# Kernel tuning notes

Measured on AMD Instinct MI355X. Metric: run time of the kernel, lower is better.

Reference implementation:

```python
import jax, jax.numpy as jnp
import numpy as np

D_MODEL = 1024
NUM_EXPERTS = 8


def setup_inputs() -> dict:
    key = jax.random.key(0)
    k_x, k_wg, k_bg, k_we, k_be = jax.random.split(key, 5)
    B, S, D, E = 4, 2048, D_MODEL, NUM_EXPERTS
    x = jax.random.normal(k_x, (B, S, D), dtype=jnp.float32)
    # gate: nn.Linear(d_model, num_experts) -> weight [E, D], bias [E]
    Wg = jax.random.normal(k_wg, (E, D), dtype=jnp.float32) * 0.02
    bg = jax.random.normal(k_bg, (E,), dtype=jnp.float32) * 0.02
    # experts: E x nn.Linear(d_model, d_model) -> weights [E, D, D], biases [E, D]
    We = jax.random.normal(k_we, (E, D, D), dtype=jnp.float32) * 0.02
    be = jax.random.normal(k_be, (E, D), dtype=jnp.float32) * 0.02
    return {"x": x, "Wg": Wg, "bg": bg, "We": We, "be": be, "top_k": 2}


def reference(x, Wg, bg, We, be, top_k):
    # gate_scores: softmax over experts. x:[B,S,D], Wg:[E,D] -> [B,S,E]
    gate_scores = jax.nn.softmax(jnp.einsum("bsd,ed->bse", x, Wg) + bg, axis=-1)
    top_k_values, top_k_indices = jax.lax.top_k(gate_scores, top_k)  # [B,S,K]
    # dense all-expert compute (faithful to original): [B,S,D,E]
    expert_outputs = jnp.einsum("bsd,ekd->bske", x, We) + be.T  # be.T: [D,E]
    # gather top-k experts along last dim: idx broadcast over feature dim D
    top_k_outputs = jnp.take_along_axis(
        expert_outputs, top_k_indices[:, :, None, :], axis=-1
    )  # [B,S,D,K]
    weighted = (top_k_outputs * top_k_values[:, :, None, :]).sum(axis=-1)  # [B,S,D]
    return weighted
```

## Files before the change

kernel.cpp:

```cpp
#include <hip/hip_runtime.h>
#include <hip/hip_bf16.h>
#include <stdint.h>

#define D_MODEL 1024
#define NUM_EXPERTS 8
#define NBUCKET 16
#define BM 128
#define BN 128
#define BK 64
#define GATE_TOK 32

typedef __bf16 bf16x8 __attribute__((ext_vector_type(8)));
typedef float f32x4 __attribute__((ext_vector_type(4)));

__device__ __forceinline__ unsigned short f32_to_bf16_rne(float f) {
    union { float f; uint32_t u; } v;
    v.f = f;
    uint32_t u = v.u;
    u += 0x7FFFu + ((u >> 16) & 1u);
    return (unsigned short)(u >> 16);
}

__device__ __forceinline__ float bf16_to_f32(unsigned short h) {
    union { uint32_t u; float f; } v;
    v.u = ((uint32_t)h) << 16;
    return v.f;
}

__device__ __forceinline__ void gload_lds16(const unsigned short* g, unsigned short* l) {
    __builtin_amdgcn_global_load_lds(
        (const __attribute__((address_space(1))) void*)g,
        (__attribute__((address_space(3))) void*)l,
        16, 0, 0);
}

__global__ __launch_bounds__(256) void gate_kernel(
    const float* __restrict__ x, const float* __restrict__ Wg,
    const float* __restrict__ bg, int T,
    int* __restrict__ counts, int* __restrict__ token_list,
    float* __restrict__ gate_list, unsigned short* __restrict__ xb)
{
    const int tid  = threadIdx.x;
    const int lane = tid & 63;
    const int wave = tid >> 6;
    const int tokBase = blockIdx.x * GATE_TOK;

    __shared__ float4 WgS[NUM_EXPERTS * 256];
    __shared__ double logitS[GATE_TOK][NUM_EXPERTS];
    __shared__ int cntS[NBUCKET];
    __shared__ int baseS[NBUCKET];

    if (tid < NBUCKET) cntS[tid] = 0;
#pragma unroll
    for (int i = 0; i < 8; i++)
        WgS[i * 256 + tid] = ((const float4*)Wg)[i * 256 + tid];
    __syncthreads();

    for (int tt = 0; tt < GATE_TOK / 4; tt++) {
        const int lt = wave * (GATE_TOK / 4) + tt;
        const int token = tokBase + lt;
        const float4* xr4 = (const float4*)(x + (size_t)token * D_MODEL);
        ushort4* xbr4 = (ushort4*)(xb + (size_t)token * D_MODEL);

        float4 xv[4];
#pragma unroll
        for (int q = 0; q < 4; q++) {
            float4 f = xr4[q * 64 + lane];
            xv[q] = f;
            ushort4 o;
            o.x = f32_to_bf16_rne(f.x);
            o.y = f32_to_bf16_rne(f.y);
            o.z = f32_to_bf16_rne(f.z);
            o.w = f32_to_bf16_rne(f.w);
            xbr4[q * 64 + lane] = o;
        }

        double acc[NUM_EXPERTS];
#pragma unroll
        for (int e = 0; e < NUM_EXPERTS; e++) {
            double a = 0.0;
#pragma unroll
            for (int q = 0; q < 4; q++) {
                float4 w = WgS[e * 256 + q * 64 + lane];
                a += (double)xv[q].x * (double)w.x;
                a += (double)xv[q].y * (double)w.y;
                a += (double)xv[q].z * (double)w.z;
                a += (double)xv[q].w * (double)w.w;
            }
            acc[e] = a;
        }
#pragma unroll
        for (int e = 0; e < NUM_EXPERTS; e++) {
            double a = acc[e];
            for (int off = 32; off > 0; off >>= 1) a += __shfl_xor(a, off, 64);
            acc[e] = a;
        }
        if (lane == 0) {
#pragma unroll
            for (int e = 0; e < NUM_EXPERTS; e++)
                logitS[lt][e] = acc[e] + (double)bg[e];
        }
    }
    __syncthreads();

    int i1 = 0, i2 = 0, o1 = 0, o2 = 0;
    double v1d = 0.0, v2d = 0.0;
    const int token2 = tokBase + tid;
    if (tid < GATE_TOK) {
        double lg[NUM_EXPERTS];
#pragma unroll
        for (int e = 0; e < NUM_EXPERTS; e++) lg[e] = logitS[tid][e];
        i1 = 0;
#pragma unroll
        for (int e = 1; e < NUM_EXPERTS; e++) if (lg[e] > lg[i1]) i1 = e;
        i2 = (i1 == 0) ? 1 : 0;
#pragma unroll
        for (int e = 0; e < NUM_EXPERTS; e++)
            if (e != i1 && lg[e] > lg[i2]) i2 = e;
        double m = lg[i1], den = 0.0;
#pragma unroll
        for (int e = 0; e < NUM_EXPERTS; e++) den += exp(lg[e] - m);
        v1d = exp(lg[i1] - m) / den;
        v2d = exp(lg[i2] - m) / den;
        o1 = atomicAdd(&cntS[i1], 1);
        o2 = atomicAdd(&cntS[8 + i2], 1);
    }
    __syncthreads();
    if (tid < NBUCKET) baseS[tid] = atomicAdd(&counts[tid], cntS[tid]);
    __syncthreads();
    if (tid < GATE_TOK) {
        int p1 = i1 * T + baseS[i1] + o1;
        token_list[p1] = token2;
        gate_list[p1]  = (float)v1d;
        int p2 = (8 + i2) * T + baseS[8 + i2] + o2;
        token_list[p2] = token2;
        gate_list[p2]  = (float)v2d;
    }
}

__global__ __launch_bounds__(256) void convert_kernel(
    const float* __restrict__ src, unsigned short* __restrict__ dst, int n4)
{
    int i = blockIdx.x * 256 + threadIdx.x;
    if (i >= n4) return;
    float4 f = ((const float4*)src)[i];
    ushort4 o;
    o.x = f32_to_bf16_rne(f.x);
    o.y = f32_to_bf16_rne(f.y);
    o.z = f32_to_bf16_rne(f.z);
    o.w = f32_to_bf16_rne(f.w);
    ((ushort4*)dst)[i] = o;
}

__global__ __launch_bounds__(256) void moe_gemm(
    const unsigned short* __restrict__ xb,
    const unsigned short* __restrict__ wb,
    const float* __restrict__ be,
    const int* __restrict__ counts,
    const int* __restrict__ token_list,
    const float* __restrict__ gate_list,
    unsigned short* __restrict__ ybuf,
    int T)
{
    const int bid = blockIdx.x;
    const int nt = bid & 7;
    const int rest = bid >> 3;
    const int vexp = rest & (NBUCKET - 1);
    const int mt = rest >> 4;
    const int e_w = vexp & 7;

    const int n_e = counts[vexp];
    const int m0 = mt * BM;
    if (m0 >= n_e) return;
    const int n0 = nt * BN;
    const int tid = threadIdx.x;

    __shared__ __align__(16) unsigned short As[BM * BK];
    __shared__ __align__(16) unsigned short Bs[BN * BK];
    __shared__ int   tokS[BM];
    __shared__ float gateS[BM];

    if (tid < BM) {
        int r = m0 + tid;
        int tk = 0; float gv = 0.f;
        if (r < n_e) {
            tk = token_list[vexp * T + r];
            gv = gate_list[vexp * T + r];
        }
        tokS[tid]  = tk;
        gateS[tid] = gv;
    }
    __syncthreads();

    const unsigned short* asrc[4];
    const unsigned short* bsrc[4];
    const unsigned short* wbase = wb + (size_t)e_w * D_MODEL * D_MODEL;
#pragma unroll
    for (int i = 0; i < 4; i++) {
        int flat = i * 256 + tid;
        int r = flat >> 3, seg = flat & 7;
        int ss = seg ^ (r & 7);
        asrc[i] = xb + (size_t)tokS[r] * D_MODEL + ss * 8;
        bsrc[i] = wbase + (size_t)(n0 + r) * D_MODEL + ss * 8;
    }

    const int wave = tid >> 6, lane = tid & 63;
    const int wm = (wave >> 1) * 64, wn = (wave & 1) * 64;
    const int frow = lane & 15;
    const int qq = lane >> 4;
    const int sw8 = frow & 7;

    f32x4 acc[4][4];
#pragma unroll
    for (int mi = 0; mi < 4; mi++)
#pragma unroll
        for (int ni = 0; ni < 4; ni++)
            acc[mi][ni] = (f32x4){0.f, 0.f, 0.f, 0.f};

    for (int kt = 0; kt < D_MODEL / BK; kt++) {
        const int k0 = kt * BK;
#pragma unroll
        for (int i = 0; i < 4; i++) {
            int flat = i * 256 + tid;
            gload_lds16(asrc[i] + k0, &As[flat * 8]);
            gload_lds16(bsrc[i] + k0, &Bs[flat * 8]);
        }
        __syncthreads();
#pragma unroll
        for (int ks = 0; ks < 2; ks++) {
            const int off = ((ks * 4 + qq) ^ sw8) * 8;
            bf16x8 af[4], bfv[4];
#pragma unroll
            for (int mi = 0; mi < 4; mi++)
                af[mi] = *(const bf16x8*)&As[(wm + mi * 16 + frow) * BK + off];
#pragma unroll
            for (int ni = 0; ni < 4; ni++)
                bfv[ni] = *(const bf16x8*)&Bs[(wn + ni * 16 + frow) * BK + off];
#pragma unroll
            for (int mi = 0; mi < 4; mi++)
#pragma unroll
                for (int ni = 0; ni < 4; ni++)
                    acc[mi][ni] = __builtin_amdgcn_mfma_f32_16x16x32_bf16(
                        af[mi], bfv[ni], acc[mi][ni], 0, 0, 0);
        }
        __syncthreads();
    }

    unsigned short* ybase = ybuf + (size_t)(vexp >> 3) * T * D_MODEL;
    const int rbase = (lane >> 4) * 4;
    const int col   = lane & 15;
#pragma unroll
    for (int mi = 0; mi < 4; mi++) {
#pragma unroll
        for (int r = 0; r < 4; r++) {
            int lrow = wm + mi * 16 + rbase + r;
            if (m0 + lrow < n_e) {
                int   tk = tokS[lrow];
                float gv = gateS[lrow];
                unsigned short* yr = ybase + (size_t)tk * D_MODEL;
#pragma unroll
                for (int ni = 0; ni < 4; ni++) {
                    int c = n0 + wn + ni * 16 + col;
                    float val = gv * (acc[mi][ni][r] + be[e_w * D_MODEL + c]);
                    yr[c] = f32_to_bf16_rne(val);
                }
            }
        }
    }
}

__global__ __launch_bounds__(256) void combine_kernel(
    const unsigned short* __restrict__ y0,
    const unsigned short* __restrict__ y1,
    float* __restrict__ out, int n4)
{
    int i = blockIdx.x * 256 + threadIdx.x;
    if (i >= n4) return;
    ushort4 a = ((const ushort4*)y0)[i];
    ushort4 b = ((const ushort4*)y1)[i];
    float4 o;
    o.x = bf16_to_f32(a.x) + bf16_to_f32(b.x);
    o.y = bf16_to_f32(a.y) + bf16_to_f32(b.y);
    o.z = bf16_to_f32(a.z) + bf16_to_f32(b.z);
    o.w = bf16_to_f32(a.w) + bf16_to_f32(b.w);
    ((float4*)out)[i] = o;
}

extern "C" void kernel_launch(void* const* d_in, const int* in_sizes, int n_in,
                              void* d_out, int out_size, void* d_ws, size_t ws_size,
                              hipStream_t stream) {
    const float* x  = (const float*)d_in[0];
    const float* Wg = (const float*)d_in[1];
    const float* bg = (const float*)d_in[2];
    const float* We = (const float*)d_in[3];
    const float* be = (const float*)d_in[4];

    const int T = in_sizes[0] / D_MODEL;

    char* ws = (char*)d_ws;
    unsigned short* xb = (unsigned short*)ws;
    size_t off = (size_t)T * D_MODEL * 2;
    unsigned short* wbv = (unsigned short*)(ws + off);
    off += (size_t)NUM_EXPERTS * D_MODEL * D_MODEL * 2;
    int* counts = (int*)(ws + off);         off += 256;
    int* token_list = (int*)(ws + off);     off += (size_t)NBUCKET * T * 4;
    float* gate_list = (float*)(ws + off);  off += (size_t)NBUCKET * T * 4;
    unsigned short* ybuf = (unsigned short*)(ws + off);
    off += (size_t)2 * T * D_MODEL * 2;

    hipMemsetAsync(counts, 0, 256, stream);

    int n4w = NUM_EXPERTS * D_MODEL * D_MODEL / 4;
    convert_kernel<<<(n4w + 255) / 256, 256, 0, stream>>>(We, wbv, n4w);

    gate_kernel<<<T / GATE_TOK, 256, 0, stream>>>(
        x, Wg, bg, T, counts, token_list, gate_list, xb);

    const int MT = (T + BM - 1) / BM;
    moe_gemm<<<MT * NBUCKET * 8, 256, 0, stream>>>(
        xb, wbv, be, counts, token_list, gate_list, ybuf, T);

    int n4c = T * D_MODEL / 4;
    combine_kernel<<<(n4c + 255) / 256, 256, 0, stream>>>(
        ybuf, ybuf + (size_t)T * D_MODEL, (float*)d_out, n4c);
}
```

Baseline: 214.9 us.

## Double-buffer GEMM LDS tiles and pre-tile expert weights into swizzled K-blocks

The weight conversion kernel now writes bf16 weights in a K-tiled, pre-swizzled layout, so each GEMM K-step reads one contiguous block of B. The GEMM keeps two LDS buffers per operand and issues the next K-tile's global-to-LDS loads before computing on the current one, aiming to hide load latency. This doubles LDS use per block, which may lower occupancy, and the trailing synchronization must still guard buffer reuse correctly.

```diff
diff --git a/kernel.cpp b/kernel.cpp
--- a/kernel.cpp
+++ b/kernel.cpp
@@ -8,10 +8,12 @@
 #define BM 128
 #define BN 128
 #define BK 64
+#define KSTEPS (D_MODEL / BK)
 #define GATE_TOK 32
 
 typedef __bf16 bf16x8 __attribute__((ext_vector_type(8)));
 typedef float f32x4 __attribute__((ext_vector_type(4)));
+typedef unsigned short u16x8 __attribute__((ext_vector_type(8)));
 
 __device__ __forceinline__ unsigned short f32_to_bf16_rne(float f) {
     union { float f; uint32_t u; } v;
@@ -139,17 +141,30 @@
 }
 
 __global__ __launch_bounds__(256) void convert_kernel(
-    const float* __restrict__ src, unsigned short* __restrict__ dst, int n4)
+    const float* __restrict__ src, unsigned short* __restrict__ dst)
 {
-    int i = blockIdx.x * 256 + threadIdx.x;
-    if (i >= n4) return;
-    float4 f = ((const float4*)src)[i];
-    ushort4 o;
-    o.x = f32_to_bf16_rne(f.x);
-    o.y = f32_to_bf16_rne(f.y);
-    o.z = f32_to_bf16_rne(f.z);
-    o.w = f32_to_bf16_rne(f.w);
-    ((ushort4*)dst)[i] = o;
+    int gid = blockIdx.x * 256 + threadIdx.x;
+    int s   = gid & 7;
+    int n   = (gid >> 3) & 1023;
+    int kt  = (gid >> 13) & (KSTEPS - 1);
+    int e   = gid >> 17;
+
+    const float* sp = src + ((size_t)(e * 1024 + n)) * 1024 + kt * BK + s * 8;
+    float4 a = ((const float4*)sp)[0];
+    float4 b = ((const float4*)sp)[1];
+    u16x8 o;
+    o[0] = f32_to_bf16_rne(a.x);
+    o[1] = f32_to_bf16_rne(a.y);
+    o[2] = f32_to_bf16_rne(a.z);
+    o[3] = f32_to_bf16_rne(a.w);
+    o[4] = f32_to_bf16_rne(b.x);
+    o[5] = f32_to_bf16_rne(b.y);
+    o[6] = f32_to_bf16_rne(b.z);
+    o[7] = f32_to_bf16_rne(b.w);
+
+    int ss = s ^ (n & 7);
+    unsigned short* dp = dst + (((size_t)(e * KSTEPS + kt) * 1024 + n) * BK) + ss * 8;
+    *(u16x8*)dp = o;
 }
 
 __global__ __launch_bounds__(256) void moe_gemm(
@@ -175,8 +190,8 @@
     const int n0 = nt * BN;
     const int tid = threadIdx.x;
 
-    __shared__ __align__(16) unsigned short As[BM * BK];
-    __shared__ __align__(16) unsigned short Bs[BN * BK];
+    __shared__ __align__(16) unsigned short As[2][BM * BK];
+    __shared__ __align__(16) unsigned short Bs[2][BN * BK];
     __shared__ int   tokS[BM];
     __shared__ float gateS[BM];
 
@@ -193,16 +208,15 @@
     __syncthreads();
 
     const unsigned short* asrc[4];
-    const unsigned short* bsrc[4];
-    const unsigned short* wbase = wb + (size_t)e_w * D_MODEL * D_MODEL;
 #pragma unroll
     for (int i = 0; i < 4; i++) {
         int flat = i * 256 + tid;
         int r = flat >> 3, seg = flat & 7;
         int ss = seg ^ (r & 7);
         asrc[i] = xb + (size_t)tokS[r] * D_MODEL + ss * 8;
-        bsrc[i] = wbase + (size_t)(n0 + r) * D_MODEL + ss * 8;
-    }
+    }
+    const unsigned short* bsrc =
+        wb + (size_t)e_w * (KSTEPS * 1024 * BK) + (size_t)n0 * BK;
 
     const int wave = tid >> 6, lane = tid & 63;
     const int wm = (wave >> 1) * 64, wn = (wave & 1) * 64;
@@ -217,25 +231,36 @@
         for (int ni = 0; ni < 4; ni++)
             acc[mi][ni] = (f32x4){0.f, 0.f, 0.f, 0.f};
 
-    for (int kt = 0; kt < D_MODEL / BK; kt++) {
-        const int k0 = kt * BK;
-#pragma unroll
-        for (int i = 0; i < 4; i++) {
-            int flat = i * 256 + tid;
-            gload_lds16(asrc[i] + k0, &As[flat * 8]);
-            gload_lds16(bsrc[i] + k0, &Bs[flat * 8]);
-        }
-        __syncthreads();
+#pragma unroll
+    for (int i = 0; i < 4; i++) {
+        int flat = i * 256 + tid;
+        gload_lds16(asrc[i], &As[0][flat * 8]);
+        gload_lds16(bsrc + flat * 8, &Bs[0][flat * 8]);
+    }
+    __syncthreads();
+
+#pragma unroll 2
+    for (int kt = 0; kt < KSTEPS; kt++) {
+        const int cur = kt & 1;
+        if (kt + 1 < KSTEPS) {
+#pragma unroll
+            for (int i = 0; i < 4; i++) {
+                int flat = i * 256 + tid;
+                gload_lds16(asrc[i] + (kt + 1) * BK, &As[cur ^ 1][flat * 8]);
+                gload_lds16(bsrc + (size_t)(kt + 1) * (1024 * BK) + flat * 8,
+                            &Bs[cur ^ 1][flat * 8]);
+            }
+        }
 #pragma unroll
         for (int ks = 0; ks < 2; ks++) {
             const int off = ((ks * 4 + qq) ^ sw8) * 8;
             bf16x8 af[4], bfv[4];
 #pragma unroll
             for (int mi = 0; mi < 4; mi++)
-                af[mi] = *(const bf16x8*)&As[(wm + mi * 16 + frow) * BK + off];
+                af[mi] = *(const bf16x8*)&As[cur][(wm + mi * 16 + frow) * BK + off];
 #pragma unroll
             for (int ni = 0; ni < 4; ni++)
-                bfv[ni] = *(const bf16x8*)&Bs[(wn + ni * 16 + frow) * BK + off];
+                bfv[ni] = *(const bf16x8*)&Bs[cur][(wn + ni * 16 + frow) * BK + off];
 #pragma unroll
             for (int mi = 0; mi < 4; mi++)
 #pragma unroll
@@ -310,8 +335,8 @@
 
     hipMemsetAsync(counts, 0, 256, stream);
 
-    int n4w = NUM_EXPERTS * D_MODEL * D_MODEL / 4;
-    convert_kernel<<<(n4w + 255) / 256, 256, 0, stream>>>(We, wbv, n4w);
+    int nseg = NUM_EXPERTS * KSTEPS * 1024 * 8;
+    convert_kernel<<<nseg / 256, 256, 0, stream>>>(We, wbv);
 
     gate_kernel<<<T / GATE_TOK, 256, 0, stream>>>(
         x, Wg, bg, T, counts, token_list, gate_list, xb);
```

Measured after the change: 214.6 us. About the same (-0.1%).
